# Kernel tuning notes

Measured on AMD Instinct MI355X. Metric: run time of the kernel, lower is better.

The kernel has to match this reference:

```python
import jax, jax.numpy as jnp
import numpy as np

B, N, D = 16, 128, 128
NEG = jnp.float32(-9e15)
LRELU_SLOPE = 0.2
HOMO_EDGES = [1, 2, 3, 4]
HETE_EDGES = [1, 5, 6, 7, 8, 9, 10]


def _mlp_proj(x, w1, b1, w2, b2):
    # Linear(D,D) -> ReLU -> Linear(D,1)
    return jax.nn.relu(x @ w1 + b1) @ w2 + b2


def setup_inputs() -> dict:
    key = jax.random.key(0)
    ks = jax.random.split(key, 16)
    s = 0.05
    return {
        "hidden": jax.random.normal(ks[0], (B, N, D), dtype=jnp.float32),
        "adj": jax.random.randint(ks[1], (B, N, N), 0, 11),
        "node_type_mask": jax.random.randint(ks[2], (B, N), 0, 4),
        "W_Q": jax.random.normal(ks[3], (4, D, D), dtype=jnp.float32) * s,
        "W_K": jax.random.normal(ks[4], (4, D, D), dtype=jnp.float32) * s,
        "W_V": jax.random.normal(ks[5], (4, D, D), dtype=jnp.float32) * s,
        "a": jax.random.normal(ks[6], (4, D), dtype=jnp.float32) * s,  # a_params, squeezed [D,1]->[D]
        "p_w1": jax.random.normal(ks[7], (D, D), dtype=jnp.float32) * s,
        "p_b1": jnp.zeros((D,), jnp.float32),
        "p_w2": jax.random.normal(ks[8], (D, 1), dtype=jnp.float32) * s,
        "p_b2": jnp.zeros((1,), jnp.float32),
        "g_w1": jax.random.normal(ks[9], (D, D), dtype=jnp.float32) * s,
        "g_b1": jnp.zeros((D,), jnp.float32),
        "g_w2": jax.random.normal(ks[10], (D, 1), dtype=jnp.float32) * s,
        "g_b2": jnp.zeros((1,), jnp.float32),
    }


def _forward(hidden, adj, node_type_mask, W_Q, W_K, W_V, a,
             p_w1, p_b1, p_w2, p_b2, g_w1, g_b1, g_w2, g_b2):
    b, n, d = hidden.shape
    flat = hidden.reshape(-1, d)                      # [B*N, D]
    mask = node_type_mask.reshape(-1)                 # [B*N]

    # typed Q projection; nodes of type 0 stay zero (matches source)
    qh = jnp.zeros_like(flat)
    for t in range(1, 4):
        qh = jnp.where((mask == t)[:, None], flat @ W_Q[t], qh)
    q = qh.reshape(b, n, d)
    # NOTE: source bug preserved — key/value are copies of query
    k = q
    v = q

    lrelu = lambda x: jax.nn.leaky_relu(x, LRELU_SLOPE)

    # ---- homo attention on value_hidden ----
    a_input = v[:, :, None, :] * v[:, None, :, :]     # [B,N,N,D] pairwise product
    alpha = jnp.full((b, n, n), NEG, dtype=hidden.dtype)
    for r in HOMO_EDGES:
        e = lrelu(jnp.einsum('bijd,d->bij', a_input, a[r - 1]))
        alpha = jnp.where(adj == r, e, alpha)
    homo_w = jax.nn.softmax(alpha, axis=-1)
    homo_output = homo_w @ v                          # [B,N,D]

    # ---- hete attention ----
    scross = jnp.einsum('bqd,bkd->bqk', q, k)         # [B,N,N]
    global_a = jnp.tanh(scross)
    global_output = global_a @ v
    scores = jnp.full_like(scross, NEG)
    for r in HETE_EDGES:
        scores = jnp.where(adj == r, scross, scores)
    scores = lrelu(scores)
    hete_w = jax.nn.softmax(scores, axis=-1)
    hete_output = hete_w @ v                          # [B,N,D]

    # ---- gate fusion ----
    input_h = jnp.stack([homo_output, hete_output], axis=-2)   # [B,N,2,D]
    energy = _mlp_proj(input_h, p_w1, p_b1, p_w2, p_b2)        # [B,N,2,1]
    w = jax.nn.softmax(energy[..., 0], axis=-1)
    local_output = (input_h * w[..., None]).sum(axis=-2)       # [B,N,D]

    input_h2 = jnp.stack([local_output, global_output], axis=-2)
    energy2 = _mlp_proj(input_h2, g_w1, g_b1, g_w2, g_b2)
    w2 = jax.nn.softmax(energy2[..., 0], axis=-1)
    attention_output = (input_h2 * w2[..., None]).sum(axis=-2)
    return attention_output


def reference(hidden, adj, node_type_mask, W_Q, W_K, W_V, a,
              p_w1, p_b1, p_w2, p_b2, g_w1, g_b1, g_w2, g_b2):
    return _forward(hidden, adj, node_type_mask, W_Q, W_K, W_V, a,
                    p_w1, p_b1, p_w2, p_b2, g_w1, g_b1, g_w2, g_b2)
```

## Files before the change

### kernel.cpp

```cpp
#include <hip/hip_runtime.h>
#include <math.h>

#define BB 16
#define NN 128
#define DD 128
#define NEGV (-9e15f)
#define SLOPE 0.2f

__global__ __launch_bounds__(128) void hete_qproj(
    const float* __restrict__ hidden, const int* __restrict__ mask,
    const float* __restrict__ WQ, float* __restrict__ q)
{
    const int r = blockIdx.x;
    const int d = threadIdx.x;
    __shared__ float h[DD];
    h[d] = hidden[r * DD + d];
    __syncthreads();
    const int t = mask[r];
    if (t == 0) { q[r * DD + d] = 0.f; return; }
    const float* W = WQ + t * DD * DD;
    float acc = 0.f;
#pragma unroll 8
    for (int k = 0; k < DD; ++k)
        acc = fmaf(h[k], W[k * DD + d], acc);
    q[r * DD + d] = acc;
}

__global__ __launch_bounds__(256) void hete_fused(
    const float* __restrict__ q, const int* __restrict__ adj,
    const float* __restrict__ aparam,
    const float* __restrict__ p_w1, const float* __restrict__ p_b1,
    const float* __restrict__ p_w2, const float* __restrict__ p_b2,
    const float* __restrict__ g_w1, const float* __restrict__ g_b1,
    const float* __restrict__ g_w2, const float* __restrict__ g_b2,
    float* __restrict__ out)
{
    __shared__ float qs[NN][DD];
    __shared__ float a_s[4][132];
    __shared__ float wrow[2][3][NN];
    __shared__ float red[4][8];
    __shared__ float enr[8];
    __shared__ __align__(16) float ro[4][3][132];

    const int tid  = threadIdx.x;
    const int b    = blockIdx.x >> 5;
    const int chunk= blockIdx.x & 31;
    const int eh   = tid >> 7;
    const int j    = tid & 127;
    const int wv   = tid >> 6;
    const int lane = tid & 63;

    const float* qb = q + b * NN * DD;
    for (int it = 0; it < (NN * DD) / 256; ++it) {
        int idx = it * 256 + tid;
        int jj = idx >> 7, dd = idx & 127;
        qs[jj][dd ^ (jj & 31)] = qb[idx];
    }
    for (int it = 0; it < 2; ++it) {
        int idx = it * 256 + tid;
        a_s[idx >> 7][idx & 127] = aparam[idx];
    }
    __syncthreads();

    for (int rp = 0; rp < 2; ++rp) {
        const int rL = rp * 2 + eh;
        const int ri = chunk * 4 + rL;
        const int adjv = adj[(b * NN + ri) * NN + j];
        const bool inH = (adjv >= 1 && adjv <= 4);
        const bool inT = (adjv == 1) || (adjv >= 5);
        const int  rh  = inH ? (adjv - 1) : 0;
        const int  risw = ri & 31;

        float s = 0.f, hm = 0.f;
#pragma unroll 4
        for (int d = 0; d < DD; ++d) {
            float qi = qs[ri][d ^ risw];
            float qj = qs[j][d ^ (j & 31)];
            float p  = qi * qj;
            s += p;
            hm = fmaf(p, a_s[rh][d], hm);
        }

        float gw = tanhf(s);
        float aH = inH ? (hm > 0.f ? hm : SLOPE * hm) : NEGV;
        float sT = inT ? s : NEGV;
        sT = (sT > 0.f) ? sT : SLOPE * sT;

        float mH = aH, mT = sT;
        for (int off = 32; off; off >>= 1) {
            mH = fmaxf(mH, __shfl_xor(mH, off));
            mT = fmaxf(mT, __shfl_xor(mT, off));
        }
        if (lane == 0) { red[wv][0] = mH; red[wv][1] = mT; }
        __syncthreads();
        mH = fmaxf(red[eh * 2][0], red[eh * 2 + 1][0]);
        mT = fmaxf(red[eh * 2][1], red[eh * 2 + 1][1]);
        float eHv = expf(aH - mH);
        float eTv = expf(sT - mT);
        float sumH = eHv, sumT = eTv;
        for (int off = 32; off; off >>= 1) {
            sumH += __shfl_xor(sumH, off);
            sumT += __shfl_xor(sumT, off);
        }
        __syncthreads();
        if (lane == 0) { red[wv][0] = sumH; red[wv][1] = sumT; }
        __syncthreads();
        sumH = red[eh * 2][0] + red[eh * 2 + 1][0];
        sumT = red[eh * 2][1] + red[eh * 2 + 1][1];
        wrow[eh][0][j] = eHv / sumH;
        wrow[eh][1][j] = eTv / sumT;
        wrow[eh][2][j] = gw;
        __syncthreads();

        const int d = j;
        float accH = 0.f, accT = 0.f, accG = 0.f;
#pragma unroll 4
        for (int jj = 0; jj < NN; ++jj) {
            float qv = qs[jj][d ^ (jj & 31)];
            accH = fmaf(wrow[eh][0][jj], qv, accH);
            accT = fmaf(wrow[eh][1][jj], qv, accT);
            accG = fmaf(wrow[eh][2][jj], qv, accG);
        }
        ro[rL][0][d] = accH;
        ro[rL][1][d] = accT;
        ro[rL][2][d] = accG;
        __syncthreads();
    }

    const int u = j;
    {
        float a0 = 0.f, a1 = 0.f, a2 = 0.f, a3 = 0.f;
        for (int k = 0; k < DD; k += 4) {
            float w0 = p_w1[(k + 0) * DD + u];
            float w1 = p_w1[(k + 1) * DD + u];
            float w2 = p_w1[(k + 2) * DD + u];
            float w3 = p_w1[(k + 3) * DD + u];
            const float4 x0 = *reinterpret_cast<const float4*>(&ro[eh * 2 + 0][0][k]);
            const float4 x1 = *reinterpret_cast<const float4*>(&ro[eh * 2 + 0][1][k]);
            const float4 x2 = *reinterpret_cast<const float4*>(&ro[eh * 2 + 1][0][k]);
            const float4 x3 = *reinterpret_cast<const float4*>(&ro[eh * 2 + 1][1][k]);
            a0 = fmaf(x0.x, w0, fmaf(x0.y, w1, fmaf(x0.z, w2, fmaf(x0.w, w3, a0))));
            a1 = fmaf(x1.x, w0, fmaf(x1.y, w1, fmaf(x1.z, w2, fmaf(x1.w, w3, a1))));
            a2 = fmaf(x2.x, w0, fmaf(x2.y, w1, fmaf(x2.z, w2, fmaf(x2.w, w3, a2))));
            a3 = fmaf(x3.x, w0, fmaf(x3.y, w1, fmaf(x3.z, w2, fmaf(x3.w, w3, a3))));
        }
        float pb1 = p_b1[u], pw2 = p_w2[u];
        float c0 = fmaxf(a0 + pb1, 0.f) * pw2;
        float c1 = fmaxf(a1 + pb1, 0.f) * pw2;
        float c2 = fmaxf(a2 + pb1, 0.f) * pw2;
        float c3 = fmaxf(a3 + pb1, 0.f) * pw2;
        for (int off = 32; off; off >>= 1) {
            c0 += __shfl_xor(c0, off);
            c1 += __shfl_xor(c1, off);
            c2 += __shfl_xor(c2, off);
            c3 += __shfl_xor(c3, off);
        }
        if (lane == 0) { red[wv][0] = c0; red[wv][1] = c1; red[wv][2] = c2; red[wv][3] = c3; }
    }
    __syncthreads();
    if (tid < 8) {
        int half = tid >> 2;
        enr[tid] = red[half * 2][tid & 3] + red[half * 2 + 1][tid & 3] + p_b2[0];
    }
    __syncthreads();
#pragma unroll
    for (int rr = 0; rr < 2; ++rr) {
        int rL = eh * 2 + rr;
        float e0 = enr[rL * 2], e1 = enr[rL * 2 + 1];
        float m  = fmaxf(e0, e1);
        float x0 = expf(e0 - m), x1 = expf(e1 - m);
        float inv = 1.f / (x0 + x1);
        ro[rL][0][u] = (x0 * ro[rL][0][u] + x1 * ro[rL][1][u]) * inv;
    }
    __syncthreads();

    {
        float a0 = 0.f, a1 = 0.f, a2 = 0.f, a3 = 0.f;
        for (int k = 0; k < DD; k += 4) {
            float w0 = g_w1[(k + 0) * DD + u];
            float w1 = g_w1[(k + 1) * DD + u];
            float w2 = g_w1[(k + 2) * DD + u];
            float w3 = g_w1[(k + 3) * DD + u];
            const float4 x0 = *reinterpret_cast<const float4*>(&ro[eh * 2 + 0][0][k]);
            const float4 x1 = *reinterpret_cast<const float4*>(&ro[eh * 2 + 0][2][k]);
            const float4 x2 = *reinterpret_cast<const float4*>(&ro[eh * 2 + 1][0][k]);
            const float4 x3 = *reinterpret_cast<const float4*>(&ro[eh * 2 + 1][2][k]);
            a0 = fmaf(x0.x, w0, fmaf(x0.y, w1, fmaf(x0.z, w2, fmaf(x0.w, w3, a0))));
            a1 = fmaf(x1.x, w0, fmaf(x1.y, w1, fmaf(x1.z, w2, fmaf(x1.w, w3, a1))));
            a2 = fmaf(x2.x, w0, fmaf(x2.y, w1, fmaf(x2.z, w2, fmaf(x2.w, w3, a2))));
            a3 = fmaf(x3.x, w0, fmaf(x3.y, w1, fmaf(x3.z, w2, fmaf(x3.w, w3, a3))));
        }
        float gb1 = g_b1[u], gw2 = g_w2[u];
        float c0 = fmaxf(a0 + gb1, 0.f) * gw2;
        float c1 = fmaxf(a1 + gb1, 0.f) * gw2;
        float c2 = fmaxf(a2 + gb1, 0.f) * gw2;
        float c3 = fmaxf(a3 + gb1, 0.f) * gw2;
        for (int off = 32; off; off >>= 1) {
            c0 += __shfl_xor(c0, off);
            c1 += __shfl_xor(c1, off);
            c2 += __shfl_xor(c2, off);
            c3 += __shfl_xor(c3, off);
        }
        __syncthreads();
        if (lane == 0) { red[wv][0] = c0; red[wv][1] = c1; red[wv][2] = c2; red[wv][3] = c3; }
    }
    __syncthreads();
    if (tid < 8) {
        int half = tid >> 2;
        enr[tid] = red[half * 2][tid & 3] + red[half * 2 + 1][tid & 3] + g_b2[0];
    }
    __syncthreads();
#pragma unroll
    for (int rr = 0; rr < 2; ++rr) {
        int rL = eh * 2 + rr;
        float e0 = enr[rL * 2], e1 = enr[rL * 2 + 1];
        float m  = fmaxf(e0, e1);
        float x0 = expf(e0 - m), x1 = expf(e1 - m);
        float inv = 1.f / (x0 + x1);
        float val = (x0 * ro[rL][0][u] + x1 * ro[rL][2][u]) * inv;
        out[(b * NN + chunk * 4 + rL) * DD + u] = val;
    }
}

extern "C" void kernel_launch(void* const* d_in, const int* in_sizes, int n_in,
                              void* d_out, int out_size, void* d_ws, size_t ws_size,
                              hipStream_t stream) {
    const float* hidden = (const float*)d_in[0];
    const int*   adj    = (const int*)d_in[1];
    const int*   mask   = (const int*)d_in[2];
    const float* W_Q    = (const float*)d_in[3];
    const float* aparam = (const float*)d_in[6];
    const float* p_w1   = (const float*)d_in[7];
    const float* p_b1   = (const float*)d_in[8];
    const float* p_w2   = (const float*)d_in[9];
    const float* p_b2   = (const float*)d_in[10];
    const float* g_w1   = (const float*)d_in[11];
    const float* g_b1   = (const float*)d_in[12];
    const float* g_w2   = (const float*)d_in[13];
    const float* g_b2   = (const float*)d_in[14];
    float* out = (float*)d_out;
    float* qws = (float*)d_ws;

    hete_qproj<<<BB * NN, 128, 0, stream>>>(hidden, mask, W_Q, qws);
    hete_fused<<<BB * 32, 256, 0, stream>>>(qws, adj, aparam,
                                            p_w1, p_b1, p_w2, p_b2,
                                            g_w1, g_b1, g_w2, g_b2, out);
}
```

Baseline: 120.2 us.

## Restructure fused attention to one row per wavefront with vectorized LDS access

Each wavefront now handles one query row and computes two columns per lane, so softmax reductions stay within a wavefront and several block-wide barriers go away. LDS loads of q, the attention vector and the softmax weights are vectorized to float4, and the output accumulation splits j across half-waves with a shuffle combine. The MLP weight matrices are staged into the reused q LDS buffer instead of being read from global memory per thread. Fast exp and tanh intrinsics replace the precise versions, which costs some accuracy.

Result: faster. 111.6 us (-7.2%).

```diff
diff --git a/kernel.cpp b/kernel.cpp
--- a/kernel.cpp
+++ b/kernel.cpp
@@ -6,6 +6,11 @@
 #define DD 128
 #define NEGV (-9e15f)
 #define SLOPE 0.2f
+
+__device__ __forceinline__ float fast_tanh(float x) {
+    float e = __expf(2.f * x);
+    return 1.f - 2.f / (e + 1.f);
+}
 
 __global__ __launch_bounds__(128) void hete_qproj(
     const float* __restrict__ hidden, const int* __restrict__ mask,
@@ -37,187 +42,233 @@
 {
     __shared__ float qs[NN][DD];
     __shared__ float a_s[4][132];
-    __shared__ float wrow[2][3][NN];
+    __shared__ float4 wreg[4][NN];
     __shared__ float red[4][8];
     __shared__ float enr[8];
-    __shared__ __align__(16) float ro[4][3][132];
-
-    const int tid  = threadIdx.x;
-    const int b    = blockIdx.x >> 5;
-    const int chunk= blockIdx.x & 31;
-    const int eh   = tid >> 7;
-    const int j    = tid & 127;
-    const int wv   = tid >> 6;
-    const int lane = tid & 63;
-
-    const float* qb = q + b * NN * DD;
-    for (int it = 0; it < (NN * DD) / 256; ++it) {
-        int idx = it * 256 + tid;
-        int jj = idx >> 7, dd = idx & 127;
-        qs[jj][dd ^ (jj & 31)] = qb[idx];
-    }
+
+    const int tid   = threadIdx.x;
+    const int b     = blockIdx.x >> 5;
+    const int chunk = blockIdx.x & 31;
+    const int wv    = tid >> 6;
+    const int lane  = tid & 63;
+    const int eh    = tid >> 7;
+    const int u     = tid & 127;
+
+    const float4* qb4 = (const float4*)(q + b * NN * DD);
+#pragma unroll
+    for (int it = 0; it < 16; ++it) {
+        int i4 = it * 256 + tid;
+        int jj = i4 >> 5, d4 = i4 & 31;
+        *(float4*)&qs[jj][(d4 ^ (jj & 31)) << 2] = qb4[i4];
+    }
+#pragma unroll
     for (int it = 0; it < 2; ++it) {
         int idx = it * 256 + tid;
         a_s[idx >> 7][idx & 127] = aparam[idx];
     }
     __syncthreads();
 
-    for (int rp = 0; rp < 2; ++rp) {
-        const int rL = rp * 2 + eh;
-        const int ri = chunk * 4 + rL;
-        const int adjv = adj[(b * NN + ri) * NN + j];
-        const bool inH = (adjv >= 1 && adjv <= 4);
-        const bool inT = (adjv == 1) || (adjv >= 5);
-        const int  rh  = inH ? (adjv - 1) : 0;
-        const int  risw = ri & 31;
-
-        float s = 0.f, hm = 0.f;
-#pragma unroll 4
-        for (int d = 0; d < DD; ++d) {
-            float qi = qs[ri][d ^ risw];
-            float qj = qs[j][d ^ (j & 31)];
-            float p  = qi * qj;
-            s += p;
-            hm = fmaf(p, a_s[rh][d], hm);
-        }
-
-        float gw = tanhf(s);
-        float aH = inH ? (hm > 0.f ? hm : SLOPE * hm) : NEGV;
-        float sT = inT ? s : NEGV;
-        sT = (sT > 0.f) ? sT : SLOPE * sT;
-
-        float mH = aH, mT = sT;
+    const int ri = chunk * 4 + wv;
+    const int j0 = lane, j1 = lane + 64;
+    const int* adjRow = adj + (b * NN + ri) * NN;
+    const int av0 = adjRow[j0], av1 = adjRow[j1];
+    const bool inH0 = (av0 >= 1) & (av0 <= 4);
+    const bool inH1 = (av1 >= 1) & (av1 <= 4);
+    const bool inT0 = (av0 == 1) | (av0 >= 5);
+    const bool inT1 = (av1 == 1) | (av1 >= 5);
+    const float* aA = &a_s[inH0 ? av0 - 1 : 0][0];
+    const float* aB = &a_s[inH1 ? av1 - 1 : 0][0];
+    const int risw = ri & 31;
+    const int jsw  = lane & 31;
+    const float* qiB = &qs[ri][0];
+    const float* qaB = &qs[j0][0];
+    const float* qbB = &qs[j1][0];
+
+    float s0 = 0.f, s1 = 0.f, hm0 = 0.f, hm1 = 0.f;
+#pragma unroll 4
+    for (int d4 = 0; d4 < 32; ++d4) {
+        float4 qi = *(const float4*)(qiB + ((d4 ^ risw) << 2));
+        float4 qa = *(const float4*)(qaB + ((d4 ^ jsw) << 2));
+        float4 qb = *(const float4*)(qbB + ((d4 ^ jsw) << 2));
+        float4 av = *(const float4*)(aA + (d4 << 2));
+        float4 bv = *(const float4*)(aB + (d4 << 2));
+        float p;
+        p = qi.x * qa.x; s0 += p; hm0 = fmaf(p, av.x, hm0);
+        p = qi.y * qa.y; s0 += p; hm0 = fmaf(p, av.y, hm0);
+        p = qi.z * qa.z; s0 += p; hm0 = fmaf(p, av.z, hm0);
+        p = qi.w * qa.w; s0 += p; hm0 = fmaf(p, av.w, hm0);
+        p = qi.x * qb.x; s1 += p; hm1 = fmaf(p, bv.x, hm1);
+        p = qi.y * qb.y; s1 += p; hm1 = fmaf(p, bv.y, hm1);
+        p = qi.z * qb.z; s1 += p; hm1 = fmaf(p, bv.z, hm1);
+        p = qi.w * qb.w; s1 += p; hm1 = fmaf(p, bv.w, hm1);
+    }
+
+    float gw0 = fast_tanh(s0), gw1 = fast_tanh(s1);
+    float aH0 = inH0 ? (hm0 > 0.f ? hm0 : SLOPE * hm0) : NEGV;
+    float aH1 = inH1 ? (hm1 > 0.f ? hm1 : SLOPE * hm1) : NEGV;
+    float t0 = inT0 ? s0 : NEGV; t0 = (t0 > 0.f) ? t0 : SLOPE * t0;
+    float t1 = inT1 ? s1 : NEGV; t1 = (t1 > 0.f) ? t1 : SLOPE * t1;
+
+    float mH = fmaxf(aH0, aH1), mT = fmaxf(t0, t1);
+#pragma unroll
+    for (int off = 32; off; off >>= 1) {
+        mH = fmaxf(mH, __shfl_xor(mH, off));
+        mT = fmaxf(mT, __shfl_xor(mT, off));
+    }
+    float eH0 = __expf(aH0 - mH), eH1 = __expf(aH1 - mH);
+    float eT0 = __expf(t0 - mT),  eT1 = __expf(t1 - mT);
+    float sH = eH0 + eH1, sT = eT0 + eT1;
+#pragma unroll
+    for (int off = 32; off; off >>= 1) {
+        sH += __shfl_xor(sH, off);
+        sT += __shfl_xor(sT, off);
+    }
+    float invH = 1.f / sH, invT = 1.f / sT;
+    wreg[wv][j0] = make_float4(eH0 * invH, eT0 * invT, gw0, 0.f);
+    wreg[wv][j1] = make_float4(eH1 * invH, eT1 * invT, gw1, 0.f);
+    __syncthreads();
+
+    const int half = lane >> 5, l5 = lane & 31;
+    float4 acH = make_float4(0,0,0,0), acT = make_float4(0,0,0,0), acG = make_float4(0,0,0,0);
+#pragma unroll 4
+    for (int jj = 0; jj < 64; ++jj) {
+        int j = half * 64 + jj;
+        float4 w4 = wreg[wv][j];
+        float4 qv = *(const float4*)(&qs[j][0] + ((l5 ^ (j & 31)) << 2));
+        acH.x = fmaf(w4.x, qv.x, acH.x); acH.y = fmaf(w4.x, qv.y, acH.y);
+        acH.z = fmaf(w4.x, qv.z, acH.z); acH.w = fmaf(w4.x, qv.w, acH.w);
+        acT.x = fmaf(w4.y, qv.x, acT.x); acT.y = fmaf(w4.y, qv.y, acT.y);
+        acT.z = fmaf(w4.y, qv.z, acT.z); acT.w = fmaf(w4.y, qv.w, acT.w);
+        acG.x = fmaf(w4.z, qv.x, acG.x); acG.y = fmaf(w4.z, qv.y, acG.y);
+        acG.z = fmaf(w4.z, qv.z, acG.z); acG.w = fmaf(w4.z, qv.w, acG.w);
+    }
+    acH.x += __shfl_xor(acH.x, 32); acH.y += __shfl_xor(acH.y, 32);
+    acH.z += __shfl_xor(acH.z, 32); acH.w += __shfl_xor(acH.w, 32);
+    acT.x += __shfl_xor(acT.x, 32); acT.y += __shfl_xor(acT.y, 32);
+    acT.z += __shfl_xor(acT.z, 32); acT.w += __shfl_xor(acT.w, 32);
+    acG.x += __shfl_xor(acG.x, 32); acG.y += __shfl_xor(acG.y, 32);
+    acG.z += __shfl_xor(acG.z, 32); acG.w += __shfl_xor(acG.w, 32);
+    {
+        float* ro = (float*)&wreg[wv][0];
+        if (half == 0) {
+            *(float4*)&ro[0 * 128 + (l5 << 2)] = acH;
+            *(float4*)&ro[1 * 128 + (l5 << 2)] = acT;
+            *(float4*)&ro[2 * 128 + (l5 << 2)] = acG;
+        }
+    }
+    __syncthreads();
+
+    float* wlds = &qs[0][0];
+    {
+        const float4* pw14 = (const float4*)p_w1;
+#pragma unroll
+        for (int it = 0; it < 16; ++it) {
+            int i4 = it * 256 + tid;
+            *(float4*)&wlds[i4 << 2] = pw14[i4];
+        }
+    }
+    __syncthreads();
+
+    const float* roA = (const float*)&wreg[eh * 2 + 0][0];
+    const float* roB = (const float*)&wreg[eh * 2 + 1][0];
+    {
+        float ga0 = 0.f, ga1 = 0.f, ga2 = 0.f, ga3 = 0.f;
+#pragma unroll 4
+        for (int k = 0; k < DD; k += 4) {
+            float w0 = wlds[(k + 0) * DD + u];
+            float w1 = wlds[(k + 1) * DD + u];
+            float w2 = wlds[(k + 2) * DD + u];
+            float w3 = wlds[(k + 3) * DD + u];
+            float4 x0 = *(const float4*)&roA[0 * 128 + k];
+            float4 x1 = *(const float4*)&roA[1 * 128 + k];
+            float4 x2 = *(const float4*)&roB[0 * 128 + k];
+            float4 x3 = *(const float4*)&roB[1 * 128 + k];
+            ga0 = fmaf(x0.x, w0, fmaf(x0.y, w1, fmaf(x0.z, w2, fmaf(x0.w, w3, ga0))));
+            ga1 = fmaf(x1.x, w0, fmaf(x1.y, w1, fmaf(x1.z, w2, fmaf(x1.w, w3, ga1))));
+            ga2 = fmaf(x2.x, w0, fmaf(x2.y, w1, fmaf(x2.z, w2, fmaf(x2.w, w3, ga2))));
+            ga3 = fmaf(x3.x, w0, fmaf(x3.y, w1, fmaf(x3.z, w2, fmaf(x3.w, w3, ga3))));
+        }
+        float pb1 = p_b1[u], pw2v = p_w2[u];
+        float c0 = fmaxf(ga0 + pb1, 0.f) * pw2v;
+        float c1 = fmaxf(ga1 + pb1, 0.f) * pw2v;
+        float c2 = fmaxf(ga2 + pb1, 0.f) * pw2v;
+        float c3 = fmaxf(ga3 + pb1, 0.f) * pw2v;
+#pragma unroll
         for (int off = 32; off; off >>= 1) {
-            mH = fmaxf(mH, __shfl_xor(mH, off));
-            mT = fmaxf(mT, __shfl_xor(mT, off));
-        }
-        if (lane == 0) { red[wv][0] = mH; red[wv][1] = mT; }
-        __syncthreads();
-        mH = fmaxf(red[eh * 2][0], red[eh * 2 + 1][0]);
-        mT = fmaxf(red[eh * 2][1], red[eh * 2 + 1][1]);
-        float eHv = expf(aH - mH);
-        float eTv = expf(sT - mT);
-        float sumH = eHv, sumT = eTv;
-        for (int off = 32; off; off >>= 1) {
-            sumH += __shfl_xor(sumH, off);
-            sumT += __shfl_xor(sumT, off);
-        }
-        __syncthreads();
-        if (lane == 0) { red[wv][0] = sumH; red[wv][1] = sumT; }
-        __syncthreads();
-        sumH = red[eh * 2][0] + red[eh * 2 + 1][0];
-        sumT = red[eh * 2][1] + red[eh * 2 + 1][1];
-        wrow[eh][0][j] = eHv / sumH;
-        wrow[eh][1][j] = eTv / sumT;
-        wrow[eh][2][j] = gw;
-        __syncthreads();
-
-        const int d = j;
-        float accH = 0.f, accT = 0.f, accG = 0.f;
-#pragma unroll 4
-        for (int jj = 0; jj < NN; ++jj) {
-            float qv = qs[jj][d ^ (jj & 31)];
-            accH = fmaf(wrow[eh][0][jj], qv, accH);
-            accT = fmaf(wrow[eh][1][jj], qv, accT);
-            accG = fmaf(wrow[eh][2][jj], qv, accG);
-        }
-        ro[rL][0][d] = accH;
-        ro[rL][1][d] = accT;
-        ro[rL][2][d] = accG;
-        __syncthreads();
-    }
-
-    const int u = j;
-    {
-        float a0 = 0.f, a1 = 0.f, a2 = 0.f, a3 = 0.f;
-        for (int k = 0; k < DD; k += 4) {
-            float w0 = p_w1[(k + 0) * DD + u];
-            float w1 = p_w1[(k + 1) * DD + u];
-            float w2 = p_w1[(k + 2) * DD + u];
-            float w3 = p_w1[(k + 3) * DD + u];
-            const float4 x0 = *reinterpret_cast<const float4*>(&ro[eh * 2 + 0][0][k]);
-            const float4 x1 = *reinterpret_cast<const float4*>(&ro[eh * 2 + 0][1][k]);
-            const float4 x2 = *reinterpret_cast<const float4*>(&ro[eh * 2 + 1][0][k]);
-            const float4 x3 = *reinterpret_cast<const float4*>(&ro[eh * 2 + 1][1][k]);
-            a0 = fmaf(x0.x, w0, fmaf(x0.y, w1, fmaf(x0.z, w2, fmaf(x0.w, w3, a0))));
-            a1 = fmaf(x1.x, w0, fmaf(x1.y, w1, fmaf(x1.z, w2, fmaf(x1.w, w3, a1))));
-            a2 = fmaf(x2.x, w0, fmaf(x2.y, w1, fmaf(x2.z, w2, fmaf(x2.w, w3, a2))));
-            a3 = fmaf(x3.x, w0, fmaf(x3.y, w1, fmaf(x3.z, w2, fmaf(x3.w, w3, a3))));
-        }
-        float pb1 = p_b1[u], pw2 = p_w2[u];
-        float c0 = fmaxf(a0 + pb1, 0.f) * pw2;
-        float c1 = fmaxf(a1 + pb1, 0.f) * pw2;
-        float c2 = fmaxf(a2 + pb1, 0.f) * pw2;
-        float c3 = fmaxf(a3 + pb1, 0.f) * pw2;
-        for (int off = 32; off; off >>= 1) {
-            c0 += __shfl_xor(c0, off);
-            c1 += __shfl_xor(c1, off);
-            c2 += __shfl_xor(c2, off);
-            c3 += __shfl_xor(c3, off);
+            c0 += __shfl_xor(c0, off); c1 += __shfl_xor(c1, off);
+            c2 += __shfl_xor(c2, off); c3 += __shfl_xor(c3, off);
         }
         if (lane == 0) { red[wv][0] = c0; red[wv][1] = c1; red[wv][2] = c2; red[wv][3] = c3; }
     }
     __syncthreads();
     if (tid < 8) {
-        int half = tid >> 2;
-        enr[tid] = red[half * 2][tid & 3] + red[half * 2 + 1][tid & 3] + p_b2[0];
+        int hf = tid >> 2;
+        enr[tid] = red[hf * 2][tid & 3] + red[hf * 2 + 1][tid & 3] + p_b2[0];
     }
     __syncthreads();
 #pragma unroll
     for (int rr = 0; rr < 2; ++rr) {
         int rL = eh * 2 + rr;
+        float* roX = (float*)&wreg[rL][0];
         float e0 = enr[rL * 2], e1 = enr[rL * 2 + 1];
-        float m  = fmaxf(e0, e1);
-        float x0 = expf(e0 - m), x1 = expf(e1 - m);
+        float m = fmaxf(e0, e1);
+        float x0 = __expf(e0 - m), x1 = __expf(e1 - m);
         float inv = 1.f / (x0 + x1);
-        ro[rL][0][u] = (x0 * ro[rL][0][u] + x1 * ro[rL][1][u]) * inv;
-    }
-    __syncthreads();
-
-    {
-        float a0 = 0.f, a1 = 0.f, a2 = 0.f, a3 = 0.f;
+        roX[0 * 128 + u] = (x0 * roX[0 * 128 + u] + x1 * roX[1 * 128 + u]) * inv;
+    }
+    {
+        const float4* gw14 = (const float4*)g_w1;
+#pragma unroll
+        for (int it = 0; it < 16; ++it) {
+            int i4 = it * 256 + tid;
+            *(float4*)&wlds[i4 << 2] = gw14[i4];
+        }
+    }
+    __syncthreads();
+    {
+        float ga0 = 0.f, ga1 = 0.f, ga2 = 0.f, ga3 = 0.f;
+#pragma unroll 4
         for (int k = 0; k < DD; k += 4) {
-            float w0 = g_w1[(k + 0) * DD + u];
-            float w1 = g_w1[(k + 1) * DD + u];
-            float w2 = g_w1[(k + 2) * DD + u];
-            float w3 = g_w1[(k + 3) * DD + u];
-            const float4 x0 = *reinterpret_cast<const float4*>(&ro[eh * 2 + 0][0][k]);
-            const float4 x1 = *reinterpret_cast<const float4*>(&ro[eh * 2 + 0][2][k]);
-            const float4 x2 = *reinterpret_cast<const float4*>(&ro[eh * 2 + 1][0][k]);
-            const float4 x3 = *reinterpret_cast<const float4*>(&ro[eh * 2 + 1][2][k]);
-            a0 = fmaf(x0.x, w0, fmaf(x0.y, w1, fmaf(x0.z, w2, fmaf(x0.w, w3, a0))));
-            a1 = fmaf(x1.x, w0, fmaf(x1.y, w1, fmaf(x1.z, w2, fmaf(x1.w, w3, a1))));
-            a2 = fmaf(x2.x, w0, fmaf(x2.y, w1, fmaf(x2.z, w2, fmaf(x2.w, w3, a2))));
-            a3 = fmaf(x3.x, w0, fmaf(x3.y, w1, fmaf(x3.z, w2, fmaf(x3.w, w3, a3))));
-        }
-        float gb1 = g_b1[u], gw2 = g_w2[u];
-        float c0 = fmaxf(a0 + gb1, 0.f) * gw2;
-        float c1 = fmaxf(a1 + gb1, 0.f) * gw2;
-        float c2 = fmaxf(a2 + gb1, 0.f) * gw2;
-        float c3 = fmaxf(a3 + gb1, 0.f) * gw2;
+            float w0 = wlds[(k + 0) * DD + u];
+            float w1 = wlds[(k + 1) * DD + u];
+            float w2 = wlds[(k + 2) * DD + u];
+            float w3 = wlds[(k + 3) * DD + u];
+            float4 x0 = *(const float4*)&roA[0 * 128 + k];
+            float4 x1 = *(const float4*)&roA[2 * 128 + k];
+            float4 x2 = *(const float4*)&roB[0 * 128 + k];
+            float4 x3 = *(const float4*)&roB[2 * 128 + k];
+            ga0 = fmaf(x0.x, w0, fmaf(x0.y, w1, fmaf(x0.z, w2, fmaf(x0.w, w3, ga0))));
+            ga1 = fmaf(x1.x, w0, fmaf(x1.y, w1, fmaf(x1.z, w2, fmaf(x1.w, w3, ga1))));
+            ga2 = fmaf(x2.x, w0, fmaf(x2.y, w1, fmaf(x2.z, w2, fmaf(x2.w, w3, ga2))));
+            ga3 = fmaf(x3.x, w0, fmaf(x3.y, w1, fmaf(x3.z, w2, fmaf(x3.w, w3, ga3))));
+        }
+        float gb1v = g_b1[u], gw2v = g_w2[u];
+        float c0 = fmaxf(ga0 + gb1v, 0.f) * gw2v;
+        float c1 = fmaxf(ga1 + gb1v, 0.f) * gw2v;
+        float c2 = fmaxf(ga2 + gb1v, 0.f) * gw2v;
+        float c3 = fmaxf(ga3 + gb1v, 0.f) * gw2v;
+#pragma unroll
         for (int off = 32; off; off >>= 1) {
-            c0 += __shfl_xor(c0, off);
-            c1 += __shfl_xor(c1, off);
-            c2 += __shfl_xor(c2, off);
-            c3 += __shfl_xor(c3, off);
-        }
-        __syncthreads();
+            c0 += __shfl_xor(c0, off); c1 += __shfl_xor(c1, off);
+            c2 += __shfl_xor(c2, off); c3 += __shfl_xor(c3, off);
+        }
         if (lane == 0) { red[wv][0] = c0; red[wv][1] = c1; red[wv][2] = c2; red[wv][3] = c3; }
     }
     __syncthreads();
     if (tid < 8) {
-        int half = tid >> 2;
-        enr[tid] = red[half * 2][tid & 3] + red[half * 2 + 1][tid & 3] + g_b2[0];
+        int hf = tid >> 2;
+        enr[tid] = red[hf * 2][tid & 3] + red[hf * 2 + 1][tid & 3] + g_b2[0];
     }
     __syncthreads();
 #pragma unroll
     for (int rr = 0; rr < 2; ++rr) {
         int rL = eh * 2 + rr;
+        const float* roX = (const float*)&wreg[rL][0];
         float e0 = enr[rL * 2], e1 = enr[rL * 2 + 1];
-        float m  = fmaxf(e0, e1);
-        float x0 = expf(e0 - m), x1 = expf(e1 - m);
+        float m = fmaxf(e0, e1);
+        float x0 = __expf(e0 - m), x1 = __expf(e1 - m);
         float inv = 1.f / (x0 + x1);
-        float val = (x0 * ro[rL][0][u] + x1 * ro[rL][2][u]) * inv;
+        float val = (x0 * roX[0 * 128 + u] + x1 * roX[2 * 128 + u]) * inv;
         out[(b * NN + chunk * 4 + rL) * DD + u] = val;
     }
 }
```
